# Kernel optimization log

Measured on AMD Instinct MI355X. Metric: run time of the kernel, lower is better.

Reference implementation:

```python
import jax, jax.numpy as jnp
import numpy as np

H, W, NUM_BINS, K = 128, 128, 32, 5
P = H * W
PAD = K // 2
EPS = 1e-5


def _gauss_kernel():
    coords = np.arange(K) - PAD
    sigma = K / 6.0
    g = np.exp(-coords ** 2 / (2 * sigma ** 2))
    g = g / g.sum()
    return jnp.asarray(np.tile(g[None, :], (P, 1)), dtype=jnp.float32)  # [P, K]


def setup_inputs() -> dict:
    key = jax.random.key(0)
    k1, k2 = jax.random.split(key)
    B, N = 8, 1000000
    u = jax.random.uniform(k1, (B, N, 4), dtype=jnp.float32)
    # columns: x in [0,H), y in [0,W), t in [0,1], polarity
    events = u * jnp.asarray([H, W, 1.0, 1.0], dtype=jnp.float32)
    bin_edges = jnp.linspace(0.0, 1.0, NUM_BINS + 1, dtype=jnp.float32)[1:-1]  # [NUM_BINS-1]
    return {
        "events": events,
        "bin_edges": bin_edges,
        "smooth_kernel": _gauss_kernel(),
        "pixel_norm_w": jnp.ones((P,), jnp.float32),
        "pixel_norm_b": jnp.zeros((P,), jnp.float32),
        "global_norm_w": jnp.ones((NUM_BINS, P), jnp.float32),
        "global_norm_b": jnp.zeros((NUM_BINS, P), jnp.float32),
    }


def _layer_norm(x, w, b, axes):
    mu = jnp.mean(x, axis=axes, keepdims=True)
    var = jnp.mean(jnp.square(x - mu), axis=axes, keepdims=True)
    return (x - mu) * jax.lax.rsqrt(var + EPS) * w + b


def _forward(events, bin_edges, smooth_kernel, pixel_norm_w, pixel_norm_b,
             global_norm_w, global_norm_b):
    B, N, _ = events.shape
    xs = jnp.clip(events[:, :, 0].astype(jnp.int32), 0, H - 1)  # [B, N]
    ys = jnp.clip(events[:, :, 1].astype(jnp.int32), 0, W - 1)
    ts = jnp.clip(events[:, :, 2], 0.0, 1.0)
    # torch.bucketize(..., right=True) == searchsorted side='right'
    bin_idx = jnp.searchsorted(bin_edges, ts, side="right").astype(jnp.int32)
    pixel_idx = xs * W + ys
    batch_offset = (jnp.arange(B, dtype=jnp.int32) * (NUM_BINS * P))[:, None]
    idx = (batch_offset + bin_idx * P + pixel_idx).reshape(-1)  # [B*N]
    counts = jnp.zeros((B * NUM_BINS * P,), jnp.float32).at[idx].add(1.0)
    spikes = counts.reshape(B, NUM_BINS, P)
    # depthwise Conv1d over the bin axis, channels = pixels
    sp = jnp.transpose(spikes, (0, 2, 1))  # [B, P, NUM_BINS]
    sp = jax.lax.conv_general_dilated(
        sp, smooth_kernel[:, None, :],  # [P, 1, K]
        window_strides=(1,), padding=[(PAD, PAD)],
        feature_group_count=P,
        dimension_numbers=("NCH", "OIH", "NCH"))
    spikes = jnp.transpose(sp, (0, 2, 1))  # [B, NUM_BINS, P]
    spikes = _layer_norm(spikes, pixel_norm_w, pixel_norm_b, axes=(-1,))
    spikes = _layer_norm(spikes, global_norm_w, global_norm_b, axes=(-2, -1))
    return spikes


def reference(events, bin_edges, smooth_kernel, pixel_norm_w, pixel_norm_b,
              global_norm_w, global_norm_b):
    return _forward(events, bin_edges, smooth_kernel, pixel_norm_w,
                    pixel_norm_b, global_norm_w, global_norm_b)
```

## Files before the change

### kernel.cpp

```cpp
#include <hip/hip_runtime.h>

#define HH 128
#define WW 128
#define PP (HH * WW)
#define NBINS 32
#define KK 5
#define PADK 2
#define EPSF 1e-5f
#define CH 4096
#define EPT 16
#define SPLITS 8
#define CPX (PP / SPLITS)
#define SLOTC 200

__device__ __forceinline__ float wave_sum(float v) {
#pragma unroll
    for (int off = 32; off > 0; off >>= 1) v += __shfl_down(v, off, 64);
    return v;
}

__global__ __launch_bounds__(256) void bucket_scatter(
    const float4* __restrict__ ev, int N, int bpb,
    unsigned short* __restrict__ buckets, unsigned short* __restrict__ lens) {
    __shared__ unsigned int cur[NBINS];
    __shared__ unsigned short sorted[NBINS * SLOTC];

    int b = blockIdx.x / bpb;
    int j = blockIdx.x - b * bpb;
    int start = j * CH;
    int nev = min(CH, N - start);
    const float4* base = ev + (size_t)b * N + start;

    if (threadIdx.x < NBINS) cur[threadIdx.x] = 0;
    __syncthreads();

#pragma unroll
    for (int k = 0; k < EPT; k++) {
        int e = threadIdx.x + k * 256;
        if (e < nev) {
            float4 q = base[e];
            int x = min(max((int)q.x, 0), HH - 1);
            int y = min(max((int)q.y, 0), WW - 1);
            float t = fminf(fmaxf(q.z, 0.0f), 1.0f);
            int bin = min((int)(t * (float)NBINS), NBINS - 1);
            unsigned int pos = atomicAdd(&cur[bin], 1u);
            if (pos < SLOTC) sorted[bin * SLOTC + pos] = (unsigned short)(x * WW + y);
        }
    }
    __syncthreads();

    if (threadIdx.x < NBINS)
        lens[(size_t)blockIdx.x * NBINS + threadIdx.x] =
            (unsigned short)min(cur[threadIdx.x], (unsigned int)SLOTC);

    for (int bin = 0; bin < NBINS; bin++) {
        unsigned int len = min(cur[bin], (unsigned int)SLOTC);
        unsigned int nw = (len + 1) >> 1;
        unsigned int* dst = (unsigned int*)(buckets +
                            ((size_t)blockIdx.x * NBINS + bin) * SLOTC);
        const unsigned int* src = (const unsigned int*)(sorted + bin * SLOTC);
        for (unsigned int w = threadIdx.x; w < nw; w += 256) dst[w] = src[w];
    }
}

__global__ __launch_bounds__(1024) void bucket_hist(
    const unsigned short* __restrict__ buckets,
    const unsigned short* __restrict__ lens, int bpb,
    unsigned short* __restrict__ counts,
    const float* __restrict__ pw, const float* __restrict__ pb,
    float* __restrict__ psums, int nParam) {
    int wave = threadIdx.x >> 6, lane = threadIdx.x & 63;

    if (blockIdx.x == (unsigned int)nParam) {
        __shared__ float pr[16][5];
        float s0 = 0, s1 = 0, s2 = 0, s3 = 0, s4 = 0;
        for (int i = threadIdx.x; i < PP / 4; i += 1024) {
            float4 w = ((const float4*)pw)[i];
            float4 b4 = ((const float4*)pb)[i];
            s0 += w.x + w.y + w.z + w.w;
            s1 += w.x * w.x + w.y * w.y + w.z * w.z + w.w * w.w;
            s2 += b4.x + b4.y + b4.z + b4.w;
            s3 += b4.x * b4.x + b4.y * b4.y + b4.z * b4.z + b4.w * b4.w;
            s4 += w.x * b4.x + w.y * b4.y + w.z * b4.z + w.w * b4.w;
        }
        float acc[5] = {s0, s1, s2, s3, s4};
#pragma unroll
        for (int q = 0; q < 5; ++q) {
            float v = wave_sum(acc[q]);
            if (lane == 0) pr[wave][q] = v;
        }
        __syncthreads();
        if (threadIdx.x < 5) {
            float t = 0.f;
            for (int w = 0; w < 16; ++w) t += pr[w][threadIdx.x];
            psums[threadIdx.x] = t;
        }
        return;
    }

    __shared__ unsigned int hist[PP / 2];
    int b = blockIdx.x >> 5;
    int bin = blockIdx.x & (NBINS - 1);

    for (int i = threadIdx.x; i < PP / 2; i += 1024) hist[i] = 0;
    __syncthreads();

    for (int j = wave; j < bpb; j += 16) {
        size_t slot = (size_t)(b * bpb + j) * NBINS + bin;
        int len = lens[slot];
        const unsigned int* src = (const unsigned int*)(buckets + slot * SLOTC);
        int nw = (len + 1) >> 1;
        for (int w = lane; w < nw; w += 64) {
            unsigned int v = src[w];
            unsigned int p0 = v & 0xFFFFu, p1 = v >> 16;
            atomicAdd(&hist[p0 >> 1], 1u << ((p0 & 1u) << 4));
            if (2 * w + 1 < len) atomicAdd(&hist[p1 >> 1], 1u << ((p1 & 1u) << 4));
        }
    }
    __syncthreads();

    unsigned int* dst = (unsigned int*)(counts + (size_t)blockIdx.x * PP);
    for (int i = threadIdx.x; i < PP / 2; i += 1024) dst[i] = hist[i];
}

__global__ __launch_bounds__(256) void conv_partials(
    const unsigned short* __restrict__ counts, const float* __restrict__ gk,
    const float* __restrict__ pw, const float* __restrict__ pb,
    float* __restrict__ partials) {
    __shared__ float red[4][8];
    int row = blockIdx.x >> 3;
    int split = blockIdx.x & (SPLITS - 1);
    int bin = row & (NBINS - 1);
    const unsigned short* base = counts + (size_t)row * PP;
    float g0 = gk[0], g1 = gk[1], g2 = gk[2], g3 = gk[3], g4 = gk[4];

    float a0 = 0, a1 = 0, a2 = 0, a3 = 0, a4 = 0, a5 = 0;

#pragma unroll
    for (int it = 0; it < CPX / (256 * 4); ++it) {
        int p = split * CPX + (it * 256 + threadIdx.x) * 4;
        float4 c[KK];
#pragma unroll
        for (int k = 0; k < KK; ++k) {
            int bb = bin + k - PADK;
            if (bb >= 0 && bb < NBINS) {
                uint2 w = *(const uint2*)(base + (ptrdiff_t)(k - PADK) * PP + p);
                c[k] = make_float4((float)(w.x & 0xFFFFu), (float)(w.x >> 16),
                                   (float)(w.y & 0xFFFFu), (float)(w.y >> 16));
            } else {
                c[k] = make_float4(0.f, 0.f, 0.f, 0.f);
            }
        }
        float4 pw4 = *(const float4*)(pw + p);
        float4 pb4 = *(const float4*)(pb + p);

        float s0 = g0*c[0].x + g1*c[1].x + g2*c[2].x + g3*c[3].x + g4*c[4].x;
        float s1 = g0*c[0].y + g1*c[1].y + g2*c[2].y + g3*c[3].y + g4*c[4].y;
        float s2 = g0*c[0].z + g1*c[1].z + g2*c[2].z + g3*c[3].z + g4*c[4].z;
        float s3 = g0*c[0].w + g1*c[1].w + g2*c[2].w + g3*c[3].w + g4*c[4].w;

        float sv[4] = {s0, s1, s2, s3};
        float wv[4] = {pw4.x, pw4.y, pw4.z, pw4.w};
        float bv[4] = {pb4.x, pb4.y, pb4.z, pb4.w};
#pragma unroll
        for (int jj = 0; jj < 4; ++jj) {
            float s = sv[jj], w = wv[jj], bb = bv[jj];
            float sw = s * w;
            a0 += s;
            a1 += s * s;
            a2 += sw;
            a3 += sw * w;
            a4 += sw * sw;
            a5 += sw * bb;
        }
    }

    float acc[6] = {a0, a1, a2, a3, a4, a5};
    int wave = threadIdx.x >> 6, lane = threadIdx.x & 63;
#pragma unroll
    for (int q = 0; q < 6; ++q) {
        float w = wave_sum(acc[q]);
        if (lane == 0) red[wave][q] = w;
    }
    __syncthreads();
    if (threadIdx.x < 6) {
        float s = red[0][threadIdx.x] + red[1][threadIdx.x] +
                  red[2][threadIdx.x] + red[3][threadIdx.x];
        partials[(size_t)blockIdx.x * 6 + threadIdx.x] = s;
    }
}

__global__ __launch_bounds__(256) void rowstats_final(
    const float* __restrict__ partials, const float* __restrict__ psums,
    float4* __restrict__ rowstats, float2* __restrict__ bstats,
    int n_rows, int B) {
    __shared__ float ys[256], ys2[256];
    float spw = psums[0], spw2 = psums[1], spb = psums[2], spb2 = psums[3],
          spwpb = psums[4];

    int t = threadIdx.x;
    float sy = 0.f, sy2 = 0.f;
    if (t < n_rows) {
        float S0 = 0, S1 = 0, S2 = 0, S3 = 0, S4 = 0, S5 = 0;
        for (int sp = 0; sp < SPLITS; ++sp) {
            const float* pp = partials + ((size_t)t * SPLITS + sp) * 6;
            S0 += pp[0]; S1 += pp[1]; S2 += pp[2];
            S3 += pp[3]; S4 += pp[4]; S5 += pp[5];
        }
        const float invP = 1.0f / (float)PP;
        float mu = S0 * invP;
        float var = S1 * invP - mu * mu;
        float rstd = rsqrtf(var + EPSF);
        sy  = rstd * (S2 - mu * spw) + spb;
        sy2 = rstd * rstd * (S4 - 2.f * mu * S3 + mu * mu * spw2)
            + 2.f * rstd * (S5 - mu * spwpb) + spb2;
        rowstats[t] = make_float4(mu, rstd, sy, sy2);
    }
    ys[t] = sy; ys2[t] = sy2;
    __syncthreads();
    if (t < B) {
        float s = 0.f, q = 0.f;
        for (int r = 0; r < NBINS; ++r) {
            s += ys[t * NBINS + r];
            q += ys2[t * NBINS + r];
        }
        const float inv = 1.0f / (float)(NBINS * PP);
        float mu = s * inv;
        float var = q * inv - mu * mu;
        bstats[t] = make_float2(mu, rsqrtf(var + EPSF));
    }
}

__global__ __launch_bounds__(256) void finalize_conv(
    const unsigned short* __restrict__ counts, const float* __restrict__ gk,
    const float* __restrict__ pw, const float* __restrict__ pb,
    const float* __restrict__ gw, const float* __restrict__ gb,
    const float4* __restrict__ rowstats, const float2* __restrict__ bstats,
    float* __restrict__ out) {
    int row = blockIdx.x >> 3;
    int split = blockIdx.x & (SPLITS - 1);
    int bin = row & (NBINS - 1);
    int b = row >> 5;
    const unsigned short* base = counts + (size_t)row * PP;
    float4 rs = rowstats[row];
    float2 bs = bstats[b];
    float g0 = gk[0], g1 = gk[1], g2 = gk[2], g3 = gk[3], g4 = gk[4];

#pragma unroll
    for (int it = 0; it < CPX / (256 * 4); ++it) {
        int p = split * CPX + (it * 256 + threadIdx.x) * 4;
        float4 c[KK];
#pragma unroll
        for (int k = 0; k < KK; ++k) {
            int bb = bin + k - PADK;
            if (bb >= 0 && bb < NBINS) {
                uint2 w = *(const uint2*)(base + (ptrdiff_t)(k - PADK) * PP + p);
                c[k] = make_float4((float)(w.x & 0xFFFFu), (float)(w.x >> 16),
                                   (float)(w.y & 0xFFFFu), (float)(w.y >> 16));
            } else {
                c[k] = make_float4(0.f, 0.f, 0.f, 0.f);
            }
        }
        float4 pw4 = *(const float4*)(pw + p);
        float4 pb4 = *(const float4*)(pb + p);
        int rp = bin * PP + p;
        float4 w4 = *(const float4*)(gw + rp);
        float4 b4 = *(const float4*)(gb + rp);

        float s0 = g0*c[0].x + g1*c[1].x + g2*c[2].x + g3*c[3].x + g4*c[4].x;
        float s1 = g0*c[0].y + g1*c[1].y + g2*c[2].y + g3*c[3].y + g4*c[4].y;
        float s2 = g0*c[0].z + g1*c[1].z + g2*c[2].z + g3*c[3].z + g4*c[4].z;
        float s3 = g0*c[0].w + g1*c[1].w + g2*c[2].w + g3*c[3].w + g4*c[4].w;

        float4 r;
        r.x = (((s0 - rs.x) * rs.y) * pw4.x + pb4.x - bs.x) * bs.y * w4.x + b4.x;
        r.y = (((s1 - rs.x) * rs.y) * pw4.y + pb4.y - bs.x) * bs.y * w4.y + b4.y;
        r.z = (((s2 - rs.x) * rs.y) * pw4.z + pb4.z - bs.x) * bs.y * w4.z + b4.z;
        r.w = (((s3 - rs.x) * rs.y) * pw4.w + pb4.w - bs.x) * bs.y * w4.w + b4.w;
        *(float4*)(out + (size_t)row * PP + p) = r;
    }
}

extern "C" void kernel_launch(void* const* d_in, const int* in_sizes, int n_in,
                              void* d_out, int out_size, void* d_ws, size_t ws_size,
                              hipStream_t stream) {
    const float* events = (const float*)d_in[0];
    const float* gk     = (const float*)d_in[2];
    const float* pw     = (const float*)d_in[3];
    const float* pb     = (const float*)d_in[4];
    const float* gw     = (const float*)d_in[5];
    const float* gb     = (const float*)d_in[6];
    float* out = (float*)d_out;

    int total_events = in_sizes[0] / 4;
    int B = out_size / (NBINS * PP);
    int N = total_events / B;
    int n_rows = B * NBINS;
    int bpb = (N + CH - 1) / CH;

    size_t count_bytes = (size_t)out_size * sizeof(unsigned short);
    char* wp = (char*)d_ws;
    unsigned short* counts = (unsigned short*)wp;  wp += count_bytes;
    float4* rowstats = (float4*)wp;             wp += (size_t)n_rows * sizeof(float4);
    float2* bstats = (float2*)wp;               wp += 64 * sizeof(float2);
    float* psums = (float*)wp;                  wp += 64 * sizeof(float);
    float* partials = (float*)wp;               wp += (size_t)n_rows * SPLITS * 6 * sizeof(float);
    unsigned short* lens = (unsigned short*)wp; wp += (size_t)B * bpb * NBINS * sizeof(unsigned short);
    wp = (char*)(((size_t)wp + 255) & ~(size_t)255);
    unsigned short* buckets = (unsigned short*)wp;

    bucket_scatter<<<B * bpb, 256, 0, stream>>>((const float4*)events, N, bpb,
                                                buckets, lens);

    bucket_hist<<<n_rows + 1, 1024, 0, stream>>>(buckets, lens, bpb, counts,
                                                 pw, pb, psums, n_rows);

    conv_partials<<<n_rows * SPLITS, 256, 0, stream>>>(counts, gk, pw, pb, partials);

    rowstats_final<<<1, 256, 0, stream>>>(partials, psums, rowstats, bstats, n_rows, B);

    finalize_conv<<<n_rows * SPLITS, 256, 0, stream>>>(counts, gk, pw, pb, gw, gb,
                                                       rowstats, bstats, out);
}
```

Measured before the change: 65.07 us.

## Fold row/batch stats into finalize kernel and use nontemporal loads/stores

```diff
diff --git a/kernel.cpp b/kernel.cpp
--- a/kernel.cpp
+++ b/kernel.cpp
@@ -13,6 +13,8 @@
 #define CPX (PP / SPLITS)
 #define SLOTC 200
 
+typedef float vfloat4 __attribute__((ext_vector_type(4)));
+
 __device__ __forceinline__ float wave_sum(float v) {
 #pragma unroll
     for (int off = 32; off > 0; off >>= 1) v += __shfl_down(v, off, 64);
@@ -29,7 +31,7 @@
     int j = blockIdx.x - b * bpb;
     int start = j * CH;
     int nev = min(CH, N - start);
-    const float4* base = ev + (size_t)b * N + start;
+    const vfloat4* base = (const vfloat4*)(ev + (size_t)b * N + start);
 
     if (threadIdx.x < NBINS) cur[threadIdx.x] = 0;
     __syncthreads();
@@ -38,7 +40,7 @@
     for (int k = 0; k < EPT; k++) {
         int e = threadIdx.x + k * 256;
         if (e < nev) {
-            float4 q = base[e];
+            vfloat4 q = __builtin_nontemporal_load(base + e);
             int x = min(max((int)q.x, 0), HH - 1);
             int y = min(max((int)q.y, 0), WW - 1);
             float t = fminf(fmaxf(q.z, 0.0f), 1.0f);
@@ -190,20 +192,26 @@
     }
 }
 
-__global__ __launch_bounds__(256) void rowstats_final(
+__global__ __launch_bounds__(256) void finalize_conv(
+    const unsigned short* __restrict__ counts, const float* __restrict__ gk,
+    const float* __restrict__ pw, const float* __restrict__ pb,
+    const float* __restrict__ gw, const float* __restrict__ gb,
     const float* __restrict__ partials, const float* __restrict__ psums,
-    float4* __restrict__ rowstats, float2* __restrict__ bstats,
-    int n_rows, int B) {
-    __shared__ float ys[256], ys2[256];
-    float spw = psums[0], spw2 = psums[1], spb = psums[2], spb2 = psums[3],
-          spwpb = psums[4];
-
+    float* __restrict__ out) {
+    __shared__ float ys[NBINS], ys2[NBINS];
+    __shared__ float sstat[4];
+    int row = blockIdx.x >> 3;
+    int split = blockIdx.x & (SPLITS - 1);
+    int bin = row & (NBINS - 1);
     int t = threadIdx.x;
-    float sy = 0.f, sy2 = 0.f;
-    if (t < n_rows) {
+
+    if (t < NBINS) {
+        float spw = psums[0], spw2 = psums[1], spb = psums[2],
+              spb2 = psums[3], spwpb = psums[4];
+        int r = (row & ~(NBINS - 1)) + t;
         float S0 = 0, S1 = 0, S2 = 0, S3 = 0, S4 = 0, S5 = 0;
         for (int sp = 0; sp < SPLITS; ++sp) {
-            const float* pp = partials + ((size_t)t * SPLITS + sp) * 6;
+            const float* pp = partials + ((size_t)r * SPLITS + sp) * 6;
             S0 += pp[0]; S1 += pp[1]; S2 += pp[2];
             S3 += pp[3]; S4 += pp[4]; S5 += pp[5];
         }
@@ -211,39 +219,25 @@
         float mu = S0 * invP;
         float var = S1 * invP - mu * mu;
         float rstd = rsqrtf(var + EPSF);
-        sy  = rstd * (S2 - mu * spw) + spb;
-        sy2 = rstd * rstd * (S4 - 2.f * mu * S3 + mu * mu * spw2)
-            + 2.f * rstd * (S5 - mu * spwpb) + spb2;
-        rowstats[t] = make_float4(mu, rstd, sy, sy2);
-    }
-    ys[t] = sy; ys2[t] = sy2;
-    __syncthreads();
-    if (t < B) {
+        ys[t]  = rstd * (S2 - mu * spw) + spb;
+        ys2[t] = rstd * rstd * (S4 - 2.f * mu * S3 + mu * mu * spw2)
+               + 2.f * rstd * (S5 - mu * spwpb) + spb2;
+        if (t == bin) { sstat[0] = mu; sstat[1] = rstd; }
+    }
+    __syncthreads();
+    if (t == 0) {
         float s = 0.f, q = 0.f;
-        for (int r = 0; r < NBINS; ++r) {
-            s += ys[t * NBINS + r];
-            q += ys2[t * NBINS + r];
-        }
+        for (int r = 0; r < NBINS; ++r) { s += ys[r]; q += ys2[r]; }
         const float inv = 1.0f / (float)(NBINS * PP);
-        float mu = s * inv;
-        float var = q * inv - mu * mu;
-        bstats[t] = make_float2(mu, rsqrtf(var + EPSF));
-    }
-}
-
-__global__ __launch_bounds__(256) void finalize_conv(
-    const unsigned short* __restrict__ counts, const float* __restrict__ gk,
-    const float* __restrict__ pw, const float* __restrict__ pb,
-    const float* __restrict__ gw, const float* __restrict__ gb,
-    const float4* __restrict__ rowstats, const float2* __restrict__ bstats,
-    float* __restrict__ out) {
-    int row = blockIdx.x >> 3;
-    int split = blockIdx.x & (SPLITS - 1);
-    int bin = row & (NBINS - 1);
-    int b = row >> 5;
+        float bmu = s * inv;
+        float bvar = q * inv - bmu * bmu;
+        sstat[2] = bmu;
+        sstat[3] = rsqrtf(bvar + EPSF);
+    }
+    __syncthreads();
+    float rmu = sstat[0], rrstd = sstat[1], bmu = sstat[2], brstd = sstat[3];
+
     const unsigned short* base = counts + (size_t)row * PP;
-    float4 rs = rowstats[row];
-    float2 bs = bstats[b];
     float g0 = gk[0], g1 = gk[1], g2 = gk[2], g3 = gk[3], g4 = gk[4];
 
 #pragma unroll
@@ -272,12 +266,12 @@
         float s2 = g0*c[0].z + g1*c[1].z + g2*c[2].z + g3*c[3].z + g4*c[4].z;
         float s3 = g0*c[0].w + g1*c[1].w + g2*c[2].w + g3*c[3].w + g4*c[4].w;
 
-        float4 r;
-        r.x = (((s0 - rs.x) * rs.y) * pw4.x + pb4.x - bs.x) * bs.y * w4.x + b4.x;
-        r.y = (((s1 - rs.x) * rs.y) * pw4.y + pb4.y - bs.x) * bs.y * w4.y + b4.y;
-        r.z = (((s2 - rs.x) * rs.y) * pw4.z + pb4.z - bs.x) * bs.y * w4.z + b4.z;
-        r.w = (((s3 - rs.x) * rs.y) * pw4.w + pb4.w - bs.x) * bs.y * w4.w + b4.w;
-        *(float4*)(out + (size_t)row * PP + p) = r;
+        vfloat4 r;
+        r.x = (((s0 - rmu) * rrstd) * pw4.x + pb4.x - bmu) * brstd * w4.x + b4.x;
+        r.y = (((s1 - rmu) * rrstd) * pw4.y + pb4.y - bmu) * brstd * w4.y + b4.y;
+        r.z = (((s2 - rmu) * rrstd) * pw4.z + pb4.z - bmu) * brstd * w4.z + b4.z;
+        r.w = (((s3 - rmu) * rrstd) * pw4.w + pb4.w - bmu) * brstd * w4.w + b4.w;
+        __builtin_nontemporal_store(r, (vfloat4*)(out + (size_t)row * PP + p));
     }
 }
 
@@ -301,8 +295,6 @@
     size_t count_bytes = (size_t)out_size * sizeof(unsigned short);
     char* wp = (char*)d_ws;
     unsigned short* counts = (unsigned short*)wp;  wp += count_bytes;
-    float4* rowstats = (float4*)wp;             wp += (size_t)n_rows * sizeof(float4);
-    float2* bstats = (float2*)wp;               wp += 64 * sizeof(float2);
     float* psums = (float*)wp;                  wp += 64 * sizeof(float);
     float* partials = (float*)wp;               wp += (size_t)n_rows * SPLITS * 6 * sizeof(float);
     unsigned short* lens = (unsigned short*)wp; wp += (size_t)B * bpb * NBINS * sizeof(unsigned short);
@@ -317,8 +309,6 @@
 
     conv_partials<<<n_rows * SPLITS, 256, 0, stream>>>(counts, gk, pw, pb, partials);
 
-    rowstats_final<<<1, 256, 0, stream>>>(partials, psums, rowstats, bstats, n_rows, B);
-
     finalize_conv<<<n_rows * SPLITS, 256, 0, stream>>>(counts, gk, pw, pb, gw, gb,
-                                                       rowstats, bstats, out);
-}
+                                                       partials, psums, out);
+}
```

Result: no change. 65.24 us (+0.3%).
